# Kernel optimization log

Measured on AMD Instinct MI355X. Metric: run time of the kernel, lower is better.

## Reference

```python
import jax, jax.numpy as jnp
import numpy as np

N = 8192
D_IN = 512
D_OUT = 128
N_EDGES = 131072
ALPHA = 0.01


def setup_inputs() -> dict:
    key = jax.random.key(0)
    ks = jax.random.split(key, 6)
    x = jax.random.normal(ks[0], (N, D_IN), dtype=jnp.float32)
    edge_index = jax.random.randint(ks[1], (2, N_EDGES), 0, N, dtype=jnp.int64)
    W1 = jax.random.normal(ks[2], (D_IN, D_OUT), dtype=jnp.float32) * (1.0 / np.sqrt(D_IN))
    b1 = jnp.zeros((D_OUT,), dtype=jnp.float32)
    W2 = jax.random.normal(ks[3], (D_IN, D_OUT), dtype=jnp.float32) * (1.0 / np.sqrt(D_IN))
    b2 = jnp.zeros((D_OUT,), dtype=jnp.float32)
    return {"x": x, "edge_index": edge_index, "W1": W1, "b1": b1, "W2": W2, "b2": b2}


def gcn_sparse(x, W, b, src, dst, n):
    # PyG GCNConv: add self loops (weight 1), symmetric D^-1/2 (A+I) D^-1/2 normalization,
    # deg computed over target index, messages src -> dst.
    h = x @ W  # [n, d_out]
    deg = jnp.zeros((n,), dtype=x.dtype).at[dst].add(1.0) + 1.0  # +1 for self loop
    dinv = jnp.where(deg > 0, 1.0 / jnp.sqrt(deg), 0.0)
    norm = dinv[src] * dinv[dst]  # [E]
    out = jnp.zeros_like(h).at[dst].add(norm[:, None] * h[src])
    out = out + (dinv * dinv)[:, None] * h  # self-loop messages
    return out + b


def gcn_dense_2hop(x, W, b, src, dst, n):
    # Mirrors high_adj: sparse A (ones, duplicates summed), A @ A, dense nonzero -> binary
    # 2-hop edges; then GCNConv on that graph (self loops appended on top of existing diag).
    A = jnp.zeros((n, n), dtype=x.dtype).at[src, dst].add(1.0)
    A2 = (A @ A > 0).astype(x.dtype)  # binary 2-hop adjacency [n, n]
    idx = jnp.arange(n)
    A2hat = A2.at[idx, idx].add(1.0)  # add_self_loops appends weight-1 self loops
    deg = A2hat.sum(axis=0)  # deg over target (column) index
    dinv = jnp.where(deg > 0, 1.0 / jnp.sqrt(deg), 0.0)
    h = x @ W
    # out[i] = dinv[i] * sum_j A2hat[j, i] * dinv[j] * h[j]
    out = dinv[:, None] * (A2hat.T @ (dinv[:, None] * h))
    return out + b


def reference(x, edge_index, W1, b1, W2, b2):
    src, dst = edge_index[0], edge_index[1]
    n = x.shape[0]
    x1 = gcn_sparse(x, W1, b1, src, dst, n)
    x2 = gcn_dense_2hop(x, W2, b2, src, dst, n)
    return jnp.concatenate([(1.0 - ALPHA) * x1, ALPHA * x2], axis=1)
```

## Files before the change

kernel.cpp:

```cpp
#include <hip/hip_runtime.h>
#include <hip/hip_bf16.h>


#define NN   8192
#define NE   131072
#define DIN  512
#define DO   128

using u64 = unsigned long long;

static constexpr size_t OFF_G1   = 0;
static constexpr size_t OFF_G2B  = OFF_G1   + 4194304;
static constexpr size_t OFF_AT   = OFF_G2B  + 2097152;
static constexpr size_t OFF_A2T  = OFF_AT   + 8388608;
static constexpr size_t OFF_CNT  = OFF_A2T  + 8388608;
static constexpr size_t OFF_FILL = OFF_CNT  + 32768;
static constexpr size_t OFF_RP   = OFF_FILL + 32768;
static constexpr size_t OFF_CSR  = OFF_RP   + 33024;
static constexpr size_t OFF_DI1  = OFF_CSR  + 524288;
static constexpr size_t OFF_DI2  = OFF_DI1  + 32768;

__device__ __forceinline__ unsigned short f2bf(float f) {
  unsigned u = __float_as_uint(f);
  return (unsigned short)((u + 0x7fffu + ((u >> 16) & 1u)) >> 16);
}


__global__ void k_zero(u64* __restrict__ AT,
                       unsigned* __restrict__ cnt, unsigned* __restrict__ fill) {
  size_t tid = (size_t)blockIdx.x * blockDim.x + threadIdx.x;
  size_t stride = (size_t)gridDim.x * blockDim.x;
  for (size_t i = tid; i < (size_t)NN * 128; i += stride) AT[i] = 0ull;
  if (tid < NN) { cnt[tid] = 0u; fill[tid] = 0u; }
}

__global__ void k_hist(const int* __restrict__ ei, unsigned* __restrict__ cnt) {
  int e = blockIdx.x * blockDim.x + threadIdx.x;
  if (e >= NE) return;
  atomicAdd(&cnt[ei[NE + e]], 1u);
}

__global__ __launch_bounds__(1024) void k_scan(const unsigned* __restrict__ cnt,
                                               unsigned* __restrict__ row_ptr,
                                               float* __restrict__ dinv1) {
  __shared__ unsigned sums[1024];
  int t = threadIdx.x;
  unsigned v[8];
  unsigned s = 0;
  #pragma unroll
  for (int i = 0; i < 8; i++) { v[i] = cnt[t * 8 + i]; s += v[i]; }
  sums[t] = s;
  __syncthreads();
  for (int off = 1; off < 1024; off *= 2) {
    unsigned add = (t >= off) ? sums[t - off] : 0u;
    __syncthreads();
    sums[t] += add;
    __syncthreads();
  }
  unsigned base = (t == 0) ? 0u : sums[t - 1];
  #pragma unroll
  for (int i = 0; i < 8; i++) {
    row_ptr[t * 8 + i] = base;
    base += v[i];
    dinv1[t * 8 + i] = rsqrtf((float)v[i] + 1.0f);
  }
  if (t == 1023) row_ptr[NN] = base;
}

__global__ void k_scatter(const int* __restrict__ ei, const unsigned* __restrict__ row_ptr,
                          unsigned* __restrict__ fill, unsigned* __restrict__ csr_src,
                          u64* __restrict__ AT) {
  int e = blockIdx.x * blockDim.x + threadIdx.x;
  if (e >= NE) return;
  int s = ei[e];
  int d = ei[NE + e];
  unsigned pos = atomicAdd(&fill[d], 1u);
  csr_src[row_ptr[d] + pos] = (unsigned)s;
  atomicOr(&AT[(size_t)d * 128 + (s >> 6)], 1ull << (s & 63));
}

__global__ __launch_bounds__(512) void k_a2t(const u64* __restrict__ AT,
                                             u64* __restrict__ A2T,
                                             float* __restrict__ dinv2) {
  const int i = blockIdx.x, t = threadIdx.x;
  __shared__ unsigned pc[128];
  __shared__ unsigned short list[512];
  __shared__ u64 redB[4][128];
  u64 w0 = 0ull;
  if (t < 128) {
    w0 = AT[(size_t)i * 128 + t];
    pc[t] = (unsigned)__popcll(w0);
  }
  __syncthreads();
  for (int off = 1; off < 128; off <<= 1) {
    unsigned add = (t >= off && t < 128) ? pc[t - off] : 0u;
    __syncthreads();
    if (t < 128) pc[t] += add;
    __syncthreads();
  }
  if (t < 128) {
    unsigned base = (t == 0) ? 0u : pc[t - 1];
    u64 m = w0;
    while (m) {
      int b = __ffsll(m) - 1;
      m &= m - 1;
      list[base++] = (unsigned short)(t * 64 + b);
    }
  }
  __syncthreads();
  const unsigned total = pc[127];
  const int q = t >> 7, c = t & 127;
  u64 acc = 0ull;
  #pragma unroll 4
  for (unsigned k = q; k < total; k += 4)
    acc |= AT[(size_t)list[k] * 128 + c];
  redB[q][c] = acc;
  __syncthreads();
  if (t < 128) {
    u64 u = redB[0][t] | redB[1][t] | redB[2][t] | redB[3][t];
    A2T[(size_t)i * 128 + t] = u;
    pc[t] = (unsigned)__popcll(u);
  }
  __syncthreads();
  for (int s = 64; s > 0; s >>= 1) {
    if (t < s) pc[t] += pc[t + s];
    __syncthreads();
  }
  if (t == 0) dinv2[i] = rsqrtf((float)pc[0] + 1.0f);
}

__global__ __launch_bounds__(256) void k_gemm(const float* __restrict__ x,
                                              const float* __restrict__ W1,
                                              const float* __restrict__ W2,
                                              const float* __restrict__ dinv1,
                                              const float* __restrict__ dinv2,
                                              float* __restrict__ g1,
                                              unsigned short* __restrict__ g2b) {
  const int bm = blockIdx.x;
  const int bn = blockIdx.y;
  const float* __restrict__ W  = (bn < 2) ? W1 : W2;
  const float* __restrict__ dv = (bn < 2) ? dinv1 : dinv2;
  const int cb = (bn & 1) * 64;
  __shared__ float As[16][68];
  __shared__ float Bs[16][64];
  const int t = threadIdx.x;
  const int tx = t & 15, ty = t >> 4;
  const int row0 = bm * 64;
  float acc[4][4] = {};
  for (int k0 = 0; k0 < DIN; k0 += 16) {
    {
      int ar = t >> 2, ak = (t & 3) * 4;
      const float4 a4 = *(const float4*)&x[(size_t)(row0 + ar) * DIN + k0 + ak];
      As[ak + 0][ar] = a4.x; As[ak + 1][ar] = a4.y;
      As[ak + 2][ar] = a4.z; As[ak + 3][ar] = a4.w;
    }
    {
      int col = t & 63, kk = t >> 6;
      #pragma unroll
      for (int u = 0; u < 4; u++, kk += 4)
        Bs[kk][col] = W[(size_t)(k0 + kk) * DO + cb + col];
    }
    __syncthreads();
    #pragma unroll
    for (int k = 0; k < 16; k++) {
      float4 a4 = *(const float4*)&As[k][ty * 4];
      float4 b4 = *(const float4*)&Bs[k][tx * 4];
      float a[4] = {a4.x, a4.y, a4.z, a4.w};
      float b[4] = {b4.x, b4.y, b4.z, b4.w};
      #pragma unroll
      for (int i = 0; i < 4; i++)
        #pragma unroll
        for (int j = 0; j < 4; j++)
          acc[i][j] += a[i] * b[j];
    }
    __syncthreads();
  }
  if (bn < 2) {
    #pragma unroll
    for (int i = 0; i < 4; i++) {
      const int r = row0 + ty * 4 + i;
      const float s = dv[r];
      float4 v = {acc[i][0] * s, acc[i][1] * s, acc[i][2] * s, acc[i][3] * s};
      *(float4*)&g1[(size_t)r * DO + cb + tx * 4] = v;
    }
  } else {
    #pragma unroll
    for (int i = 0; i < 4; i++) {
      const int r = row0 + ty * 4 + i;
      const float s = dv[r];
      ushort4 v = {f2bf(acc[i][0] * s), f2bf(acc[i][1] * s),
                   f2bf(acc[i][2] * s), f2bf(acc[i][3] * s)};
      *(ushort4*)&g2b[(size_t)r * DO + cb + tx * 4] = v;
    }
  }
}

__global__ __launch_bounds__(256) void k_spmm1(const float* __restrict__ g1,
                                               const unsigned* __restrict__ row_ptr,
                                               const unsigned* __restrict__ csr_src,
                                               const float* __restrict__ dinv1,
                                               const float* __restrict__ b1,
                                               float* __restrict__ out) {
  const int i = blockIdx.x, t = threadIdx.x;
  __shared__ float redA[4][128];
  const int q = t >> 6, c = t & 63;
  const unsigned lo = row_ptr[i], hi = row_ptr[i + 1];
  float a0 = 0.f, a1 = 0.f;
  #pragma unroll 4
  for (unsigned e = lo + q; e < hi; e += 4) {
    unsigned j = csr_src[e];
    float2 v = *(const float2*)&g1[(size_t)j * DO + 2 * c];
    a0 += v.x; a1 += v.y;
  }
  redA[q][2 * c] = a0;
  redA[q][2 * c + 1] = a1;
  __syncthreads();
  if (t < 128) {
    float s = redA[0][t] + redA[1][t] + redA[2][t] + redA[3][t]
            + g1[(size_t)i * DO + t];
    out[(size_t)i * 256 + t] = 0.99f * (dinv1[i] * s + b1[t]);
  }
}

__global__ __launch_bounds__(256) void k_spmm2(const unsigned short* __restrict__ g2b,
                                               const u64* __restrict__ A2T,
                                               const float* __restrict__ dinv2,
                                               const float* __restrict__ b2,
                                               float* __restrict__ out) {
  const int i = blockIdx.x, t = threadIdx.x;
  __shared__ unsigned pc[128];
  __shared__ unsigned short list[8192];
  __shared__ float redA[4][128];
  u64 w0 = 0ull;
  if (t < 128) {
    w0 = A2T[(size_t)i * 128 + t];
    pc[t] = (unsigned)__popcll(w0);
  }
  __syncthreads();
  for (int off = 1; off < 128; off <<= 1) {
    unsigned add = (t >= off && t < 128) ? pc[t - off] : 0u;
    __syncthreads();
    if (t < 128) pc[t] += add;
    __syncthreads();
  }
  if (t < 128) {
    unsigned base = (t == 0) ? 0u : pc[t - 1];
    u64 m = w0;
    while (m) {
      int b = __ffsll(m) - 1;
      m &= m - 1;
      list[base++] = (unsigned short)(t * 64 + b);
    }
  }
  __syncthreads();
  const unsigned total = pc[127];
  const int q = t >> 6, c = t & 63;
  float a0 = 0.f, a1 = 0.f;
  #pragma unroll 4
  for (unsigned k = q; k < total; k += 4) {
    unsigned j = list[k];
    unsigned u = *(const unsigned*)&g2b[(size_t)j * DO + 2 * c];
    a0 += __uint_as_float(u << 16);
    a1 += __uint_as_float(u & 0xffff0000u);
  }
  redA[q][2 * c] = a0;
  redA[q][2 * c + 1] = a1;
  __syncthreads();
  if (t < 128) {
    unsigned us = g2b[(size_t)i * DO + t];
    float self = __uint_as_float((unsigned)us << 16);
    float s = redA[0][t] + redA[1][t] + redA[2][t] + redA[3][t] + self;
    out[(size_t)i * 256 + 128 + t] = 0.01f * (dinv2[i] * s + b2[t]);
  }
}


extern "C" void kernel_launch(void* const* d_in, const int* in_sizes, int n_in,
                              void* d_out, int out_size, void* d_ws, size_t ws_size,
                              hipStream_t stream) {
  const float* x  = (const float*)d_in[0];
  const int*   ei = (const int*)d_in[1];
  const float* W1 = (const float*)d_in[2];
  const float* b1 = (const float*)d_in[3];
  const float* W2 = (const float*)d_in[4];
  const float* b2 = (const float*)d_in[5];
  float* out = (float*)d_out;
  char* ws = (char*)d_ws;

  float* g1              = (float*)(ws + OFF_G1);
  unsigned short* g2b    = (unsigned short*)(ws + OFF_G2B);
  u64* AT                = (u64*)(ws + OFF_AT);
  u64* A2T               = (u64*)(ws + OFF_A2T);
  unsigned* cnt          = (unsigned*)(ws + OFF_CNT);
  unsigned* fill         = (unsigned*)(ws + OFF_FILL);
  unsigned* row_ptr      = (unsigned*)(ws + OFF_RP);
  unsigned* csr_src      = (unsigned*)(ws + OFF_CSR);
  float* dinv1           = (float*)(ws + OFF_DI1);
  float* dinv2           = (float*)(ws + OFF_DI2);

  k_zero<<<1024, 256, 0, stream>>>(AT, cnt, fill);
  k_hist<<<NE / 256, 256, 0, stream>>>(ei, cnt);
  k_scan<<<1, 1024, 0, stream>>>(cnt, row_ptr, dinv1);
  k_scatter<<<NE / 256, 256, 0, stream>>>(ei, row_ptr, fill, csr_src, AT);
  k_a2t<<<NN, 512, 0, stream>>>(AT, A2T, dinv2);
  dim3 gg(NN / 64, 4);
  k_gemm<<<gg, 256, 0, stream>>>(x, W1, W2, dinv1, dinv2, g1, g2b);
  k_spmm1<<<NN, 256, 0, stream>>>(g1, row_ptr, csr_src, dinv1, b1, out);
  k_spmm2<<<NN, 256, 0, stream>>>(g2b, A2T, dinv2, b2, out);
}
```

Before: 209.6 us.

## Use bf16 MFMA with split-bf16 emulation for GEMM and widen SpMM blocks

Replaces the FP32 SIMT GEMM with a bf16 MFMA GEMM. For the W1 branch it uses a split hi/lo bf16 decomposition (xh*Wh + xh*Wl + xl*Wh) over an extended K of 1536 to keep near-fp32 accuracy, while the W2 branch uses plain bf16. Adds conversion kernels for x and the weights, and loads tiles with global_load_lds into LDS. The SpMM kernels move to 512 threads with 8 partial-sum lanes to add memory-level parallelism. The cost is extra passes to convert x and an additional 16MB of workspace traffic.

Result: slower. 218.5 us (+4.3%).

```diff
diff --git a/kernel.cpp b/kernel.cpp
--- a/kernel.cpp
+++ b/kernel.cpp
@@ -8,12 +8,17 @@
 #define DO   128
 
 using u64 = unsigned long long;
+typedef __attribute__((ext_vector_type(8))) short short8v;
+typedef __attribute__((ext_vector_type(4))) float f32x4;
 
 static constexpr size_t OFF_G1   = 0;
 static constexpr size_t OFF_G2B  = OFF_G1   + 4194304;
 static constexpr size_t OFF_AT   = OFF_G2B  + 2097152;
 static constexpr size_t OFF_A2T  = OFF_AT   + 8388608;
-static constexpr size_t OFF_CNT  = OFF_A2T  + 8388608;
+static constexpr size_t OFF_XH   = OFF_A2T  + 8388608;
+static constexpr size_t OFF_XL   = OFF_XH   + 8388608;
+static constexpr size_t OFF_BT   = OFF_XL   + 8388608;
+static constexpr size_t OFF_CNT  = OFF_BT   + 786432;
 static constexpr size_t OFF_FILL = OFF_CNT  + 32768;
 static constexpr size_t OFF_RP   = OFF_FILL + 32768;
 static constexpr size_t OFF_CSR  = OFF_RP   + 33024;
@@ -23,6 +28,13 @@
 __device__ __forceinline__ unsigned short f2bf(float f) {
   unsigned u = __float_as_uint(f);
   return (unsigned short)((u + 0x7fffu + ((u >> 16) & 1u)) >> 16);
+}
+__device__ __forceinline__ float bf2f(unsigned short h) {
+  return __uint_as_float((unsigned)h << 16);
+}
+__device__ __forceinline__ void load_lds16(const void* g, void* l) {
+  __builtin_amdgcn_global_load_lds((const __attribute__((address_space(1))) void*)g,
+                                   (__attribute__((address_space(3))) void*)l, 16, 0, 0);
 }
 
 
@@ -129,85 +141,132 @@
   if (t == 0) dinv2[i] = rsqrtf((float)pc[0] + 1.0f);
 }
 
-__global__ __launch_bounds__(256) void k_gemm(const float* __restrict__ x,
-                                              const float* __restrict__ W1,
-                                              const float* __restrict__ W2,
+__global__ void k_conv(const float* __restrict__ x, unsigned short* __restrict__ xh,
+                       unsigned short* __restrict__ xl) {
+  size_t i = (size_t)blockIdx.x * blockDim.x + threadIdx.x;
+  size_t stride = (size_t)gridDim.x * blockDim.x;
+  for (size_t p = i; p < (size_t)NN * DIN / 4; p += stride) {
+    float4 v = ((const float4*)x)[p];
+    ushort4 h, l;
+    h.x = f2bf(v.x); l.x = f2bf(v.x - bf2f(h.x));
+    h.y = f2bf(v.y); l.y = f2bf(v.y - bf2f(h.y));
+    h.z = f2bf(v.z); l.z = f2bf(v.z - bf2f(h.z));
+    h.w = f2bf(v.w); l.w = f2bf(v.w - bf2f(h.w));
+    ((ushort4*)xh)[p] = h;
+    ((ushort4*)xl)[p] = l;
+  }
+}
+
+__global__ __launch_bounds__(256) void k_bprep(const float* __restrict__ W1,
+                                               const float* __restrict__ W2,
+                                               unsigned short* __restrict__ Bt) {
+  const int t = blockIdx.x * 256 + threadIdx.x;
+  if (t >= 8192) return;
+  const int n = t & 127, kb = (t >> 7) << 3;
+  short8v vh, vl, v2;
+  #pragma unroll
+  for (int j = 0; j < 8; j++) {
+    float w = W1[(size_t)(kb + j) * DO + n];
+    unsigned short h = f2bf(w);
+    vh[j] = (short)h;
+    vl[j] = (short)f2bf(w - bf2f(h));
+    v2[j] = (short)f2bf(W2[(size_t)(kb + j) * DO + n]);
+  }
+  unsigned short* r1 = &Bt[(size_t)n * 1536];
+  *(short8v*)&r1[kb]        = vh;
+  *(short8v*)&r1[512 + kb]  = vl;
+  *(short8v*)&r1[1024 + kb] = vh;
+  *(short8v*)&Bt[(size_t)(128 + n) * 1536 + kb] = v2;
+}
+
+__global__ __launch_bounds__(256) void k_gemm(const unsigned short* __restrict__ xh,
+                                              const unsigned short* __restrict__ xl,
+                                              const unsigned short* __restrict__ Bt,
                                               const float* __restrict__ dinv1,
                                               const float* __restrict__ dinv2,
                                               float* __restrict__ g1,
                                               unsigned short* __restrict__ g2b) {
-  const int bm = blockIdx.x;
-  const int bn = blockIdx.y;
-  const float* __restrict__ W  = (bn < 2) ? W1 : W2;
-  const float* __restrict__ dv = (bn < 2) ? dinv1 : dinv2;
-  const int cb = (bn & 1) * 64;
-  __shared__ float As[16][68];
-  __shared__ float Bs[16][64];
-  const int t = threadIdx.x;
-  const int tx = t & 15, ty = t >> 4;
-  const int row0 = bm * 64;
-  float acc[4][4] = {};
-  for (int k0 = 0; k0 < DIN; k0 += 16) {
-    {
-      int ar = t >> 2, ak = (t & 3) * 4;
-      const float4 a4 = *(const float4*)&x[(size_t)(row0 + ar) * DIN + k0 + ak];
-      As[ak + 0][ar] = a4.x; As[ak + 1][ar] = a4.y;
-      As[ak + 2][ar] = a4.z; As[ak + 3][ar] = a4.w;
+  const int bm = blockIdx.x, bn = blockIdx.y;
+  const int Kext = (bn < 2) ? 1536 : 512;
+  __shared__ __align__(16) unsigned short As[4096];
+  __shared__ __align__(16) unsigned short Bs[4096];
+  const int tid = threadIdx.x;
+  const int lane = tid & 63, wv = tid >> 6;
+  const int wr = wv >> 1, wc = wv & 1;
+
+  const int c0 = tid, c1 = tid + 256;
+  const int cb0 = c0 >> 6, l0 = c0 & 63;
+  const int cb1 = c1 >> 6, l1 = c1 & 63;
+  const int rT0 = (cb0 >> 1) * 16 + (l0 & 15), kc0 = (cb0 & 1) * 4 + (l0 >> 4);
+  const int rT1 = (cb1 >> 1) * 16 + (l1 & 15), kc1 = (cb1 & 1) * 4 + (l1 >> 4);
+  const size_t gA0 = (size_t)(bm * 64 + rT0) * DIN + kc0 * 8;
+  const size_t gA1 = (size_t)(bm * 64 + rT1) * DIN + kc1 * 8;
+  const size_t gB0 = (size_t)(bn * 64 + rT0) * 1536 + kc0 * 8;
+  const size_t gB1 = (size_t)(bn * 64 + rT1) * 1536 + kc1 * 8;
+
+  const int lofs = lane * 8;
+
+  f32x4 acc00 = {0.f, 0.f, 0.f, 0.f};
+  f32x4 acc01 = acc00, acc10 = acc00, acc11 = acc00;
+
+  for (int k0 = 0; k0 < Kext; k0 += 64) {
+    const unsigned short* sA =
+        (k0 < 512) ? (xh + k0) : (k0 < 1024) ? (xh + (k0 - 512)) : (xl + (k0 - 1024));
+    load_lds16(sA + gA0, &As[c0 * 8]);
+    load_lds16(sA + gA1, &As[c1 * 8]);
+    load_lds16(Bt + k0 + gB0, &Bs[c0 * 8]);
+    load_lds16(Bt + k0 + gB1, &Bs[c1 * 8]);
+    __syncthreads();
+    #pragma unroll
+    for (int ks = 0; ks < 2; ks++) {
+      short8v a0 = *(const short8v*)&As[(wr * 4 + ks) * 512 + lofs];
+      short8v a1 = *(const short8v*)&As[(wr * 4 + 2 + ks) * 512 + lofs];
+      short8v b0 = *(const short8v*)&Bs[(wc * 4 + ks) * 512 + lofs];
+      short8v b1 = *(const short8v*)&Bs[(wc * 4 + 2 + ks) * 512 + lofs];
+      acc00 = __builtin_amdgcn_mfma_f32_16x16x32_bf16(a0, b0, acc00, 0, 0, 0);
+      acc01 = __builtin_amdgcn_mfma_f32_16x16x32_bf16(a0, b1, acc01, 0, 0, 0);
+      acc10 = __builtin_amdgcn_mfma_f32_16x16x32_bf16(a1, b0, acc10, 0, 0, 0);
+      acc11 = __builtin_amdgcn_mfma_f32_16x16x32_bf16(a1, b1, acc11, 0, 0, 0);
     }
-    {
-      int col = t & 63, kk = t >> 6;
+    __syncthreads();
+  }
+
+  const int colb = lane & 15;
+  const int rowb = (lane >> 4) << 2;
+  #pragma unroll
+  for (int m = 0; m < 2; m++) {
+    #pragma unroll
+    for (int n = 0; n < 2; n++) {
+      f32x4 a = (m == 0) ? (n == 0 ? acc00 : acc01) : (n == 0 ? acc10 : acc11);
+      const int cl = wc * 32 + n * 16 + colb;
       #pragma unroll
-      for (int u = 0; u < 4; u++, kk += 4)
-        Bs[kk][col] = W[(size_t)(k0 + kk) * DO + cb + col];
+      for (int r = 0; r < 4; r++) {
+        const int gr = bm * 64 + wr * 32 + m * 16 + rowb + r;
+        if (bn < 2) {
+          const int gc = bn * 64 + cl;
+          g1[(size_t)gr * DO + gc] = dinv1[gr] * a[r];
+        } else {
+          const int gc = (bn - 2) * 64 + cl;
+          g2b[(size_t)gr * DO + gc] = f2bf(dinv2[gr] * a[r]);
+        }
+      }
     }
-    __syncthreads();
-    #pragma unroll
-    for (int k = 0; k < 16; k++) {
-      float4 a4 = *(const float4*)&As[k][ty * 4];
-      float4 b4 = *(const float4*)&Bs[k][tx * 4];
-      float a[4] = {a4.x, a4.y, a4.z, a4.w};
-      float b[4] = {b4.x, b4.y, b4.z, b4.w};
-      #pragma unroll
-      for (int i = 0; i < 4; i++)
-        #pragma unroll
-        for (int j = 0; j < 4; j++)
-          acc[i][j] += a[i] * b[j];
-    }
-    __syncthreads();
-  }
-  if (bn < 2) {
-    #pragma unroll
-    for (int i = 0; i < 4; i++) {
-      const int r = row0 + ty * 4 + i;
-      const float s = dv[r];
-      float4 v = {acc[i][0] * s, acc[i][1] * s, acc[i][2] * s, acc[i][3] * s};
-      *(float4*)&g1[(size_t)r * DO + cb + tx * 4] = v;
-    }
-  } else {
-    #pragma unroll
-    for (int i = 0; i < 4; i++) {
-      const int r = row0 + ty * 4 + i;
-      const float s = dv[r];
-      ushort4 v = {f2bf(acc[i][0] * s), f2bf(acc[i][1] * s),
-                   f2bf(acc[i][2] * s), f2bf(acc[i][3] * s)};
-      *(ushort4*)&g2b[(size_t)r * DO + cb + tx * 4] = v;
-    }
-  }
-}
-
-__global__ __launch_bounds__(256) void k_spmm1(const float* __restrict__ g1,
+  }
+}
+
+__global__ __launch_bounds__(512) void k_spmm1(const float* __restrict__ g1,
                                                const unsigned* __restrict__ row_ptr,
                                                const unsigned* __restrict__ csr_src,
                                                const float* __restrict__ dinv1,
                                                const float* __restrict__ b1,
                                                float* __restrict__ out) {
   const int i = blockIdx.x, t = threadIdx.x;
-  __shared__ float redA[4][128];
+  __shared__ float redA[8][128];
   const int q = t >> 6, c = t & 63;
   const unsigned lo = row_ptr[i], hi = row_ptr[i + 1];
   float a0 = 0.f, a1 = 0.f;
-  #pragma unroll 4
-  for (unsigned e = lo + q; e < hi; e += 4) {
+  #pragma unroll 2
+  for (unsigned e = lo + q; e < hi; e += 8) {
     unsigned j = csr_src[e];
     float2 v = *(const float2*)&g1[(size_t)j * DO + 2 * c];
     a0 += v.x; a1 += v.y;
@@ -216,13 +275,14 @@
   redA[q][2 * c + 1] = a1;
   __syncthreads();
   if (t < 128) {
-    float s = redA[0][t] + redA[1][t] + redA[2][t] + redA[3][t]
-            + g1[(size_t)i * DO + t];
+    float s = g1[(size_t)i * DO + t];
+    #pragma unroll
+    for (int r = 0; r < 8; r++) s += redA[r][t];
     out[(size_t)i * 256 + t] = 0.99f * (dinv1[i] * s + b1[t]);
   }
 }
 
-__global__ __launch_bounds__(256) void k_spmm2(const unsigned short* __restrict__ g2b,
+__global__ __launch_bounds__(512) void k_spmm2(const unsigned short* __restrict__ g2b,
                                                const u64* __restrict__ A2T,
                                                const float* __restrict__ dinv2,
                                                const float* __restrict__ b2,
@@ -230,7 +290,7 @@
   const int i = blockIdx.x, t = threadIdx.x;
   __shared__ unsigned pc[128];
   __shared__ unsigned short list[8192];
-  __shared__ float redA[4][128];
+  __shared__ float redA[8][128];
   u64 w0 = 0ull;
   if (t < 128) {
     w0 = A2T[(size_t)i * 128 + t];
@@ -257,7 +317,7 @@
   const int q = t >> 6, c = t & 63;
   float a0 = 0.f, a1 = 0.f;
   #pragma unroll 4
-  for (unsigned k = q; k < total; k += 4) {
+  for (unsigned k = q; k < total; k += 8) {
     unsigned j = list[k];
     unsigned u = *(const unsigned*)&g2b[(size_t)j * DO + 2 * c];
     a0 += __uint_as_float(u << 16);
@@ -267,9 +327,9 @@
   redA[q][2 * c + 1] = a1;
   __syncthreads();
   if (t < 128) {
-    unsigned us = g2b[(size_t)i * DO + t];
-    float self = __uint_as_float((unsigned)us << 16);
-    float s = redA[0][t] + redA[1][t] + redA[2][t] + redA[3][t] + self;
+    float s = bf2f(g2b[(size_t)i * DO + t]);
+    #pragma unroll
+    for (int r = 0; r < 8; r++) s += redA[r][t];
     out[(size_t)i * 256 + 128 + t] = 0.01f * (dinv2[i] * s + b2[t]);
   }
 }
@@ -291,6 +351,9 @@
   unsigned short* g2b    = (unsigned short*)(ws + OFF_G2B);
   u64* AT                = (u64*)(ws + OFF_AT);
   u64* A2T               = (u64*)(ws + OFF_A2T);
+  unsigned short* xh     = (unsigned short*)(ws + OFF_XH);
+  unsigned short* xl     = (unsigned short*)(ws + OFF_XL);
+  unsigned short* Bt     = (unsigned short*)(ws + OFF_BT);
   unsigned* cnt          = (unsigned*)(ws + OFF_CNT);
   unsigned* fill         = (unsigned*)(ws + OFF_FILL);
   unsigned* row_ptr      = (unsigned*)(ws + OFF_RP);
@@ -303,8 +366,10 @@
   k_scan<<<1, 1024, 0, stream>>>(cnt, row_ptr, dinv1);
   k_scatter<<<NE / 256, 256, 0, stream>>>(ei, row_ptr, fill, csr_src, AT);
   k_a2t<<<NN, 512, 0, stream>>>(AT, A2T, dinv2);
+  k_conv<<<2048, 256, 0, stream>>>(x, xh, xl);
+  k_bprep<<<32, 256, 0, stream>>>(W1, W2, Bt);
   dim3 gg(NN / 64, 4);
-  k_gemm<<<gg, 256, 0, stream>>>(x, W1, W2, dinv1, dinv2, g1, g2b);
-  k_spmm1<<<NN, 256, 0, stream>>>(g1, row_ptr, csr_src, dinv1, b1, out);
-  k_spmm2<<<NN, 256, 0, stream>>>(g2b, A2T, dinv2, b2, out);
-}
+  k_gemm<<<gg, 256, 0, stream>>>(xh, xl, Bt, dinv1, dinv2, g1, g2b);
+  k_spmm1<<<NN, 512, 0, stream>>>(g1, row_ptr, csr_src, dinv1, b1, out);
+  k_spmm2<<<NN, 512, 0, stream>>>(g2b, A2T, dinv2, b2, out);
+}
```
